# Kernel tuning notes

Measured on AMD Instinct MI355X. Metric: run time of the kernel, lower is better.

Reference implementation:

```python
import jax, jax.numpy as jnp
import numpy as np

B = 2
T = 1024
D_MODEL = 1024
EXPAND = 2
D_INNER = D_MODEL * EXPAND  # 2048
D_STATE = 16
D_CONV = 4
DT_RANK = 64  # ceil(1024/16)


def setup_inputs() -> dict:
    key = jax.random.key(0)
    ks = jax.random.split(key, 9)
    s = 0.02
    x = jax.random.normal(ks[0], (B, T, D_MODEL), jnp.float32)
    in_proj_w = jax.random.normal(ks[1], (2 * D_INNER, D_MODEL), jnp.float32) * s
    conv_w = jax.random.normal(ks[2], (D_INNER, 1, D_CONV), jnp.float32) * 0.1
    conv_b = jax.random.normal(ks[3], (D_INNER,), jnp.float32) * 0.01
    x_proj_w = jax.random.normal(ks[4], (DT_RANK + 2 * D_STATE, D_INNER), jnp.float32) * s
    dt_proj_w = jax.random.normal(ks[5], (D_INNER, DT_RANK), jnp.float32) * s
    dt_proj_b = jax.random.uniform(ks[6], (D_INNER,), jnp.float32, -4.0, -2.0)
    A_log = jnp.log(jnp.tile(jnp.arange(1, D_STATE + 1, dtype=jnp.float32), (D_INNER, 1)))
    D_param = jnp.ones((D_INNER,), jnp.float32)
    out_proj_w = jax.random.normal(ks[7], (D_MODEL, D_INNER), jnp.float32) * s
    return {"x": x, "in_proj_w": in_proj_w, "conv_w": conv_w, "conv_b": conv_b,
            "x_proj_w": x_proj_w, "dt_proj_w": dt_proj_w, "dt_proj_b": dt_proj_b,
            "A_log": A_log, "D_param": D_param, "out_proj_w": out_proj_w}


def reference(x, in_proj_w, conv_w, conv_b, x_proj_w, dt_proj_w, dt_proj_b,
              A_log, D_param, out_proj_w):
    Bsz, Tlen, _ = x.shape
    # input projection -> (B,T,2*d_inner); split into x-branch and gate z
    xz = jnp.einsum('btd,ed->bte', x, in_proj_w)
    xs, z = jnp.split(xz, 2, axis=-1)
    # causal depthwise conv1d: torch pads both sides by d_conv-1 then slices [:T],
    # equivalent to left-pad d_conv-1
    xc = jnp.swapaxes(xs, 1, 2)  # (B, d_inner, T)
    xc = jax.lax.conv_general_dilated(xc, conv_w, window_strides=(1,),
                                      padding=[(D_CONV - 1, 0)],
                                      feature_group_count=D_INNER)
    xc = xc + conv_b[None, :, None]
    xs = jax.nn.silu(jnp.swapaxes(xc, 1, 2))  # (B,T,d_inner)
    A = -jnp.exp(A_log)  # (d_inner, d_state)
    x_dbl = jnp.einsum('bti,ei->bte', xs, x_proj_w)
    dt, Bv, Cv = jnp.split(x_dbl, [DT_RANK, DT_RANK + D_STATE], axis=-1)
    dt = jax.nn.softplus(jnp.einsum('btr,ir->bti', dt, dt_proj_w) + dt_proj_b)
    # selective scan: h_t = exp(dt_t*A)*h_{t-1} + (dt_t*x_t)*B_t ; y_t = <h_t, C_t>
    def step(h, inp):
        dt_t, B_t, C_t, x_t = inp  # (B,Di),(B,Ds),(B,Ds),(B,Di)
        dA = jnp.exp(dt_t[:, :, None] * A[None])        # (B,Di,Ds)
        h = dA * h + (dt_t * x_t)[:, :, None] * B_t[:, None, :]
        y_t = jnp.einsum('bds,bs->bd', h, C_t)
        return h, y_t
    tm = lambda a: jnp.swapaxes(a, 0, 1)  # time-major
    h0 = jnp.zeros((Bsz, D_INNER, D_STATE), x.dtype)
    _, ys = jax.lax.scan(step, h0, (tm(dt), tm(Bv), tm(Cv), tm(xs)))
    y = jnp.swapaxes(ys, 0, 1) + xs * D_param  # (B,T,d_inner)
    y = y * jax.nn.silu(z)
    return jnp.einsum('bti,di->btd', y, out_proj_w)
```

## Files before the change

### kernel.cpp

```cpp
#include <hip/hip_runtime.h>
#include <hip/hip_bf16.h>
#include <math.h>

#define B_SZ 2
#define T_LEN 1024
#define DMODEL 1024
#define DINNER 2048
#define DSTATE 16
#define DCONV 4
#define DTRANK 64
#define MTOK (B_SZ * T_LEN)

#define NC 32
#define CLEN (T_LEN / NC)
#define NCH (B_SZ * DINNER)
#define NSTATES (NCH * DSTATE)

typedef __bf16 bf16x4 __attribute__((ext_vector_type(4)));
typedef __bf16 bf16x8 __attribute__((ext_vector_type(8)));
typedef float  f32x4  __attribute__((ext_vector_type(4)));

__device__ __forceinline__ float sigmoid_f(float v) { return 1.f / (1.f + __expf(-v)); }

__global__ __launch_bounds__(256) void convert_f32_bf16(const float* __restrict__ src,
                                                        __bf16* __restrict__ dst)
{
    const int i = blockIdx.x * blockDim.x + threadIdx.x;
    float4 a = reinterpret_cast<const float4*>(src)[2 * i];
    float4 b = reinterpret_cast<const float4*>(src)[2 * i + 1];
    bf16x8 o = {(__bf16)a.x, (__bf16)a.y, (__bf16)a.z, (__bf16)a.w,
                (__bf16)b.x, (__bf16)b.y, (__bf16)b.z, (__bf16)b.w};
    reinterpret_cast<bf16x8*>(dst)[i] = o;
}

template<int BN>
__global__ __launch_bounds__(256) void mfma_gemm_bf16(const __bf16* __restrict__ A, int lda,
                                                      const __bf16* __restrict__ Bm, int ldb,
                                                      float* __restrict__ C, int ldc, int K)
{
    constexpr int NF = BN / 32;
    constexpr int BCALLS = BN / 32;
    __shared__ __align__(16) __bf16 As[128 * 64];
    __shared__ __align__(16) __bf16 Bs[BN * 64];
    const int tid  = threadIdx.x;
    const int lane = tid & 63;
    const int w    = tid >> 6;
    const int wr   = w >> 1, wc = w & 1;
    const int m0   = blockIdx.y * 128, n0 = blockIdx.x * BN;

    f32x4 acc[4][NF];
    #pragma unroll
    for (int i = 0; i < 4; ++i)
        #pragma unroll
        for (int j = 0; j < NF; ++j) {
            f32x4 z = {0.f, 0.f, 0.f, 0.f};
            acc[i][j] = z;
        }

    const int fr = lane & 15;
    const int kq = (lane >> 4) * 8;

    for (int k0 = 0; k0 < K; k0 += 64) {
        #pragma unroll
        for (int c = 0; c < 4; ++c) {
            const int idx = c * 256 + tid;
            const int row = idx >> 3;
            const int kc  = (idx & 7) * 8;
            __builtin_amdgcn_global_load_lds(
                (const __attribute__((address_space(1))) unsigned int*)(A + (size_t)(m0 + row) * lda + k0 + kc),
                (__attribute__((address_space(3))) unsigned int*)(As + idx * 8),
                16, 0, 0);
        }
        #pragma unroll
        for (int c = 0; c < BCALLS; ++c) {
            const int idx = c * 256 + tid;
            const int row = idx >> 3;
            const int kc  = (idx & 7) * 8;
            __builtin_amdgcn_global_load_lds(
                (const __attribute__((address_space(1))) unsigned int*)(Bm + (size_t)(n0 + row) * ldb + k0 + kc),
                (__attribute__((address_space(3))) unsigned int*)(Bs + idx * 8),
                16, 0, 0);
        }
        __syncthreads();

        bf16x8 af[4][2], bfr[NF][2];
        #pragma unroll
        for (int i = 0; i < 4; ++i) {
            const __bf16* pa = As + (wr * 64 + i * 16 + fr) * 64 + kq;
            af[i][0] = *reinterpret_cast<const bf16x8*>(pa);
            af[i][1] = *reinterpret_cast<const bf16x8*>(pa + 32);
        }
        #pragma unroll
        for (int j = 0; j < NF; ++j) {
            const __bf16* pb = Bs + (wc * (BN / 2) + j * 16 + fr) * 64 + kq;
            bfr[j][0] = *reinterpret_cast<const bf16x8*>(pb);
            bfr[j][1] = *reinterpret_cast<const bf16x8*>(pb + 32);
        }
        #pragma unroll
        for (int i = 0; i < 4; ++i)
            #pragma unroll
            for (int j = 0; j < NF; ++j) {
                acc[i][j] = __builtin_amdgcn_mfma_f32_16x16x32_bf16(af[i][0], bfr[j][0], acc[i][j], 0, 0, 0);
                acc[i][j] = __builtin_amdgcn_mfma_f32_16x16x32_bf16(af[i][1], bfr[j][1], acc[i][j], 0, 0, 0);
            }
        __syncthreads();
    }

    const int crow = (lane >> 4) * 4;
    const int ccol = lane & 15;
    #pragma unroll
    for (int i = 0; i < 4; ++i)
        #pragma unroll
        for (int j = 0; j < NF; ++j) {
            float* cp = C + (size_t)(m0 + wr * 64 + i * 16 + crow) * ldc
                          + n0 + wc * (BN / 2) + j * 16 + ccol;
            cp[0 * ldc] = acc[i][j][0];
            cp[1 * ldc] = acc[i][j][1];
            cp[2 * ldc] = acc[i][j][2];
            cp[3 * ldc] = acc[i][j][3];
        }
}

template<int EPI>
__global__ __launch_bounds__(256) void gemm_nt(const float* __restrict__ A, int lda,
                                               const float* __restrict__ Bm, int ldb,
                                               float* __restrict__ C, int ldc,
                                               int M, int N, int K,
                                               const float* __restrict__ bias)
{
    __shared__ float As[16][68];
    __shared__ float Bs[16][68];
    const int tx = threadIdx.x & 15;
    const int ty = threadIdx.x >> 4;
    const int m0 = blockIdx.y * 64;
    const int n0 = blockIdx.x * 64;
    const int lr = threadIdx.x >> 2;
    const int lc = (threadIdx.x & 3) * 4;

    float acc[4][4] = {};

    for (int k0 = 0; k0 < K; k0 += 16) {
        {
            int m = m0 + lr;
            float4 v = make_float4(0.f, 0.f, 0.f, 0.f);
            if (m < M) v = *reinterpret_cast<const float4*>(&A[(size_t)m * lda + k0 + lc]);
            As[lc + 0][lr] = v.x; As[lc + 1][lr] = v.y;
            As[lc + 2][lr] = v.z; As[lc + 3][lr] = v.w;
        }
        {
            int n = n0 + lr;
            float4 v = make_float4(0.f, 0.f, 0.f, 0.f);
            if (n < N) v = *reinterpret_cast<const float4*>(&Bm[(size_t)n * ldb + k0 + lc]);
            Bs[lc + 0][lr] = v.x; Bs[lc + 1][lr] = v.y;
            Bs[lc + 2][lr] = v.z; Bs[lc + 3][lr] = v.w;
        }
        __syncthreads();
        #pragma unroll
        for (int kk = 0; kk < 16; ++kk) {
            float av[4], bv[4];
            #pragma unroll
            for (int i = 0; i < 4; ++i) av[i] = As[kk][ty + 16 * i];
            #pragma unroll
            for (int j = 0; j < 4; ++j) bv[j] = Bs[kk][tx + 16 * j];
            #pragma unroll
            for (int i = 0; i < 4; ++i)
                #pragma unroll
                for (int j = 0; j < 4; ++j)
                    acc[i][j] = fmaf(av[i], bv[j], acc[i][j]);
        }
        __syncthreads();
    }

    #pragma unroll
    for (int i = 0; i < 4; ++i) {
        int m = m0 + ty + 16 * i;
        if (m >= M) continue;
        #pragma unroll
        for (int j = 0; j < 4; ++j) {
            int n = n0 + tx + 16 * j;
            if (n >= N) continue;
            float v = acc[i][j];
            if (EPI == 1) {
                v += bias[n];
                v = (v > 20.f) ? v : log1pf(__expf(v));
            }
            C[(size_t)m * ldc + n] = v;
        }
    }
}

#define XP_KS 16
#define XP_KC (DINNER / XP_KS)

__global__ __launch_bounds__(256) void gemm_xproj_splitk(const float* __restrict__ xs,
                                                         const float* __restrict__ W,
                                                         float* __restrict__ pbuf)
{
    __shared__ float As[16][68];
    __shared__ float Bs[16][68];
    const int tx = threadIdx.x & 15;
    const int ty = threadIdx.x >> 4;
    const int n0 = blockIdx.x * 64;
    const int m0 = blockIdx.y * 64;
    const int kz = blockIdx.z;
    const int lr = threadIdx.x >> 2;
    const int lc = (threadIdx.x & 3) * 4;

    float acc[4][4] = {};

    for (int k0 = kz * XP_KC; k0 < (kz + 1) * XP_KC; k0 += 16) {
        {
            float4 v = *reinterpret_cast<const float4*>(&xs[(size_t)(m0 + lr) * DINNER + k0 + lc]);
            As[lc + 0][lr] = v.x; As[lc + 1][lr] = v.y;
            As[lc + 2][lr] = v.z; As[lc + 3][lr] = v.w;
        }
        {
            int n = n0 + lr;
            float4 v = make_float4(0.f, 0.f, 0.f, 0.f);
            if (n < DTRANK + 2 * DSTATE)
                v = *reinterpret_cast<const float4*>(&W[(size_t)n * DINNER + k0 + lc]);
            Bs[lc + 0][lr] = v.x; Bs[lc + 1][lr] = v.y;
            Bs[lc + 2][lr] = v.z; Bs[lc + 3][lr] = v.w;
        }
        __syncthreads();
        #pragma unroll
        for (int kk = 0; kk < 16; ++kk) {
            float av[4], bv[4];
            #pragma unroll
            for (int i = 0; i < 4; ++i) av[i] = As[kk][ty + 16 * i];
            #pragma unroll
            for (int j = 0; j < 4; ++j) bv[j] = Bs[kk][tx + 16 * j];
            #pragma unroll
            for (int i = 0; i < 4; ++i)
                #pragma unroll
                for (int j = 0; j < 4; ++j)
                    acc[i][j] = fmaf(av[i], bv[j], acc[i][j]);
        }
        __syncthreads();
    }

    float* pc = pbuf + (size_t)kz * MTOK * 96;
    #pragma unroll
    for (int i = 0; i < 4; ++i) {
        int m = m0 + ty + 16 * i;
        #pragma unroll
        for (int j = 0; j < 4; ++j) {
            int n = n0 + tx + 16 * j;
            if (n < 96) pc[(size_t)m * 96 + n] = acc[i][j];
        }
    }
}

__global__ __launch_bounds__(256) void reduce_xproj(const float* __restrict__ pbuf,
                                                    float* __restrict__ xdbl)
{
    const int idx = blockIdx.x * blockDim.x + threadIdx.x;
    const float4* p = reinterpret_cast<const float4*>(pbuf) + idx;
    float4 s = p[0];
    #pragma unroll
    for (int z = 1; z < XP_KS; ++z) {
        float4 v = p[(size_t)z * (MTOK * 96 / 4)];
        s.x += v.x; s.y += v.y; s.z += v.z; s.w += v.w;
    }
    reinterpret_cast<float4*>(xdbl)[idx] = s;
}

__global__ __launch_bounds__(256) void conv_silu_kernel(const float* __restrict__ xz,
                                                        const float* __restrict__ cw,
                                                        const float* __restrict__ cb,
                                                        float* __restrict__ xs)
{
    int tid = blockIdx.x * blockDim.x + threadIdx.x;
    int d = tid & (DINNER - 1);
    int t = (tid >> 11) & (T_LEN - 1);
    int b = tid >> 21;
    float acc = cb[d];
    const float4 w = *reinterpret_cast<const float4*>(&cw[d * DCONV]);
    float wv[4] = {w.x, w.y, w.z, w.w};
    #pragma unroll
    for (int j = 0; j < DCONV; ++j) {
        int tt = t - (DCONV - 1) + j;
        if (tt >= 0)
            acc = fmaf(xz[((size_t)(b * T_LEN + tt)) * (2 * DINNER) + d], wv[j], acc);
    }
    xs[tid] = acc * sigmoid_f(acc);
}

__global__ __launch_bounds__(256) void scan_pass1(const float* __restrict__ dt,
                                                  const float* __restrict__ xs,
                                                  const float* __restrict__ xdbl,
                                                  const float* __restrict__ A_log,
                                                  float* __restrict__ Pb,
                                                  float* __restrict__ Bb)
{
    __shared__ float sB[CLEN][16];
    const int tid = threadIdx.x;
    const int g   = blockIdx.x * 256 + tid;
    const int c   = blockIdx.y;
    const int b   = g >> 11;
    const int d   = g & (DINNER - 1);
    const int m0  = b * T_LEN + c * CLEN;

    if (tid < CLEN * 4) {
        int t = tid >> 2, s4 = (tid & 3) * 4;
        *reinterpret_cast<float4*>(&sB[t][s4]) =
            *reinterpret_cast<const float4*>(&xdbl[(size_t)(m0 + t) * 96 + DTRANK + s4]);
    }
    __syncthreads();

    float a[DSTATE], h[DSTATE];
    #pragma unroll
    for (int s4 = 0; s4 < DSTATE; s4 += 4) {
        float4 v = *reinterpret_cast<const float4*>(&A_log[d * DSTATE + s4]);
        a[s4 + 0] = -__expf(v.x); a[s4 + 1] = -__expf(v.y);
        a[s4 + 2] = -__expf(v.z); a[s4 + 3] = -__expf(v.w);
        h[s4 + 0] = 0.f; h[s4 + 1] = 0.f; h[s4 + 2] = 0.f; h[s4 + 3] = 0.f;
    }

    float sumdt = 0.f;
    float dtc = dt[(size_t)m0 * DINNER + d];
    float xc  = xs[(size_t)m0 * DINNER + d];
    for (int t = 0; t < CLEN; ++t) {
        float dtn = 0.f, xn = 0.f;
        if (t + 1 < CLEN) {
            dtn = dt[(size_t)(m0 + t + 1) * DINNER + d];
            xn  = xs[(size_t)(m0 + t + 1) * DINNER + d];
        }
        sumdt += dtc;
        const float u = dtc * xc;
        #pragma unroll
        for (int s = 0; s < DSTATE; ++s) {
            const float dA = __expf(dtc * a[s]);
            h[s] = fmaf(dA, h[s], u * sB[t][s]);
        }
        dtc = dtn; xc = xn;
    }

    float* pp = Pb + ((size_t)c * NCH + g) * DSTATE;
    float* bp = Bb + ((size_t)c * NCH + g) * DSTATE;
    #pragma unroll
    for (int s4 = 0; s4 < DSTATE; s4 += 4) {
        float4 pv = {__expf(a[s4] * sumdt), __expf(a[s4 + 1] * sumdt),
                     __expf(a[s4 + 2] * sumdt), __expf(a[s4 + 3] * sumdt)};
        *reinterpret_cast<float4*>(pp + s4) = pv;
        float4 hv = {h[s4], h[s4 + 1], h[s4 + 2], h[s4 + 3]};
        *reinterpret_cast<float4*>(bp + s4) = hv;
    }
}

__global__ __launch_bounds__(256) void scan_pass2(const float* __restrict__ Pb,
                                                  float* __restrict__ Bb)
{
    const int idx = blockIdx.x * blockDim.x + threadIdx.x;
    float h = 0.f;
    #pragma unroll
    for (int c = 0; c < NC; ++c) {
        const size_t o = (size_t)c * NSTATES + idx;
        const float P  = Pb[o];
        const float Bv = Bb[o];
        Bb[o] = h;
        h = fmaf(P, h, Bv);
    }
}

__global__ __launch_bounds__(256) void scan_pass3(const float* __restrict__ dt,
                                                  const float* __restrict__ xs,
                                                  const float* __restrict__ xdbl,
                                                  const float* __restrict__ Hs,
                                                  const float* __restrict__ A_log,
                                                  const float* __restrict__ Dp,
                                                  const float* __restrict__ xz,
                                                  __bf16* __restrict__ yMb)
{
    __shared__ float sBC[CLEN][32];
    const int tid = threadIdx.x;
    const int g   = blockIdx.x * 256 + tid;
    const int c   = blockIdx.y;
    const int b   = g >> 11;
    const int d   = g & (DINNER - 1);
    const int m0  = b * T_LEN + c * CLEN;

    {
        int t = tid >> 3, col = (tid & 7) * 4;
        if (t < CLEN)
            *reinterpret_cast<float4*>(&sBC[t][col]) =
                *reinterpret_cast<const float4*>(&xdbl[(size_t)(m0 + t) * 96 + DTRANK + col]);
    }
    __syncthreads();

    float a[DSTATE], h[DSTATE];
    #pragma unroll
    for (int s4 = 0; s4 < DSTATE; s4 += 4) {
        float4 v = *reinterpret_cast<const float4*>(&A_log[d * DSTATE + s4]);
        a[s4 + 0] = -__expf(v.x); a[s4 + 1] = -__expf(v.y);
        a[s4 + 2] = -__expf(v.z); a[s4 + 3] = -__expf(v.w);
        float4 hv = *reinterpret_cast<const float4*>(
            Hs + ((size_t)c * NCH + g) * DSTATE + s4);
        h[s4 + 0] = hv.x; h[s4 + 1] = hv.y; h[s4 + 2] = hv.z; h[s4 + 3] = hv.w;
    }
    const float Dv = Dp[d];

    float dtc = dt[(size_t)m0 * DINNER + d];
    float xc  = xs[(size_t)m0 * DINNER + d];
    float zc  = xz[(size_t)m0 * (2 * DINNER) + DINNER + d];
    for (int t = 0; t < CLEN; ++t) {
        float dtn = 0.f, xn = 0.f, zn = 0.f;
        if (t + 1 < CLEN) {
            dtn = dt[(size_t)(m0 + t + 1) * DINNER + d];
            xn  = xs[(size_t)(m0 + t + 1) * DINNER + d];
            zn  = xz[(size_t)(m0 + t + 1) * (2 * DINNER) + DINNER + d];
        }
        const float u = dtc * xc;
        float y0 = 0.f, y1 = 0.f, y2 = 0.f, y3 = 0.f;
        #pragma unroll
        for (int s = 0; s < DSTATE; s += 4) {
            float dA0 = __expf(dtc * a[s + 0]);
            float dA1 = __expf(dtc * a[s + 1]);
            float dA2 = __expf(dtc * a[s + 2]);
            float dA3 = __expf(dtc * a[s + 3]);
            h[s + 0] = fmaf(dA0, h[s + 0], u * sBC[t][s + 0]);
            h[s + 1] = fmaf(dA1, h[s + 1], u * sBC[t][s + 1]);
            h[s + 2] = fmaf(dA2, h[s + 2], u * sBC[t][s + 2]);
            h[s + 3] = fmaf(dA3, h[s + 3], u * sBC[t][s + 3]);
            y0 = fmaf(h[s + 0], sBC[t][16 + s + 0], y0);
            y1 = fmaf(h[s + 1], sBC[t][16 + s + 1], y1);
            y2 = fmaf(h[s + 2], sBC[t][16 + s + 2], y2);
            y3 = fmaf(h[s + 3], sBC[t][16 + s + 3], y3);
        }
        float y = (y0 + y1) + (y2 + y3) + xc * Dv;
        const float gate = zc * sigmoid_f(zc);
        yMb[(size_t)(m0 + t) * DINNER + d] = (__bf16)(y * gate);
        dtc = dtn; xc = xn; zc = zn;
    }
}

extern "C" void kernel_launch(void* const* d_in, const int* in_sizes, int n_in,
                              void* d_out, int out_size, void* d_ws, size_t ws_size,
                              hipStream_t stream) {
    const float* x         = (const float*)d_in[0];
    const float* in_proj_w = (const float*)d_in[1];
    const float* conv_w    = (const float*)d_in[2];
    const float* conv_b    = (const float*)d_in[3];
    const float* x_proj_w  = (const float*)d_in[4];
    const float* dt_proj_w = (const float*)d_in[5];
    const float* dt_proj_b = (const float*)d_in[6];
    const float* A_log     = (const float*)d_in[7];
    const float* D_param   = (const float*)d_in[8];
    const float* out_proj_w= (const float*)d_in[9];
    float* out = (float*)d_out;

    float* ws   = (float*)d_ws;
    const size_t M1 = (size_t)1024 * 1024;
    float*  xz     = ws;
    float*  xs     = ws + 8 * M1;
    __bf16* xb     = (__bf16*)(ws + 8 * M1);
    __bf16* wb_in  = (__bf16*)(ws + 9 * M1);
    float*  dt     = ws + 12 * M1;
    __bf16* wb_out = (__bf16*)(ws + 12 * M1);
    float*  pbuf   = ws + 16 * M1;
    float*  Pb     = ws + 16 * M1;
    float*  Bb     = ws + 18 * M1;
    __bf16* yMb    = (__bf16*)(ws + 16 * M1);
    float*  xdbl   = ws + 20 * M1;

    dim3 blk(256);

    convert_f32_bf16<<<dim3(MTOK * DMODEL / 8 / 256), blk, 0, stream>>>(x, xb);
    convert_f32_bf16<<<dim3(2 * DINNER * DMODEL / 8 / 256), blk, 0, stream>>>(in_proj_w, wb_in);

    mfma_gemm_bf16<128><<<dim3((2 * DINNER) / 128, MTOK / 128), blk, 0, stream>>>(
        xb, DMODEL, wb_in, DMODEL, xz, 2 * DINNER, DMODEL);

    conv_silu_kernel<<<dim3(B_SZ * T_LEN * DINNER / 256), blk, 0, stream>>>(xz, conv_w, conv_b, xs);

    gemm_xproj_splitk<<<dim3(2, MTOK / 64, XP_KS), blk, 0, stream>>>(xs, x_proj_w, pbuf);

    reduce_xproj<<<dim3(MTOK * 96 / 4 / 256), blk, 0, stream>>>(pbuf, xdbl);

    gemm_nt<1><<<dim3(DINNER / 64, MTOK / 64), blk, 0, stream>>>(
        xdbl, 96, dt_proj_w, DTRANK, dt, DINNER, MTOK, DINNER, DTRANK, dt_proj_b);

    scan_pass1<<<dim3(NCH / 256, NC), blk, 0, stream>>>(dt, xs, xdbl, A_log, Pb, Bb);
    scan_pass2<<<dim3(NSTATES / 256), blk, 0, stream>>>(Pb, Bb);
    scan_pass3<<<dim3(NCH / 256, NC), blk, 0, stream>>>(dt, xs, xdbl, Bb, A_log, D_param, xz, yMb);

    convert_f32_bf16<<<dim3(DMODEL * DINNER / 8 / 256), blk, 0, stream>>>(out_proj_w, wb_out);

    mfma_gemm_bf16<64><<<dim3(DMODEL / 64, MTOK / 128), blk, 0, stream>>>(
        yMb, DINNER, wb_out, DINNER, out, DMODEL, DINNER);
}
```

Before: 202.9 us.

## Store intermediates in bf16 and merge the three conversion kernels

```diff
diff --git a/kernel.cpp b/kernel.cpp
--- a/kernel.cpp
+++ b/kernel.cpp
@@ -22,21 +22,29 @@
 
 __device__ __forceinline__ float sigmoid_f(float v) { return 1.f / (1.f + __expf(-v)); }
 
-__global__ __launch_bounds__(256) void convert_f32_bf16(const float* __restrict__ src,
-                                                        __bf16* __restrict__ dst)
-{
-    const int i = blockIdx.x * blockDim.x + threadIdx.x;
-    float4 a = reinterpret_cast<const float4*>(src)[2 * i];
-    float4 b = reinterpret_cast<const float4*>(src)[2 * i + 1];
-    bf16x8 o = {(__bf16)a.x, (__bf16)a.y, (__bf16)a.z, (__bf16)a.w,
+__global__ __launch_bounds__(256) void convert3(const float* __restrict__ x,
+                                                const float* __restrict__ w_in,
+                                                const float* __restrict__ w_out,
+                                                __bf16* __restrict__ xb,
+                                                __bf16* __restrict__ wb_in,
+                                                __bf16* __restrict__ wb_out)
+{
+    const int gi = blockIdx.x * blockDim.x + threadIdx.x;
+    const float* src; __bf16* dst; int o;
+    if (gi < 262144)            { src = x;     dst = xb;     o = gi; }
+    else if (gi < 786432)       { src = w_in;  dst = wb_in;  o = gi - 262144; }
+    else                        { src = w_out; dst = wb_out; o = gi - 786432; }
+    float4 a = reinterpret_cast<const float4*>(src)[2 * o];
+    float4 b = reinterpret_cast<const float4*>(src)[2 * o + 1];
+    bf16x8 v = {(__bf16)a.x, (__bf16)a.y, (__bf16)a.z, (__bf16)a.w,
                 (__bf16)b.x, (__bf16)b.y, (__bf16)b.z, (__bf16)b.w};
-    reinterpret_cast<bf16x8*>(dst)[i] = o;
-}
-
-template<int BN>
+    reinterpret_cast<bf16x8*>(dst)[o] = v;
+}
+
+template<int BN, typename CT>
 __global__ __launch_bounds__(256) void mfma_gemm_bf16(const __bf16* __restrict__ A, int lda,
                                                       const __bf16* __restrict__ Bm, int ldb,
-                                                      float* __restrict__ C, int ldc, int K)
+                                                      CT* __restrict__ C, int ldc, int K)
 {
     constexpr int NF = BN / 32;
     constexpr int BCALLS = BN / 32;
@@ -112,21 +120,19 @@
     for (int i = 0; i < 4; ++i)
         #pragma unroll
         for (int j = 0; j < NF; ++j) {
-            float* cp = C + (size_t)(m0 + wr * 64 + i * 16 + crow) * ldc
-                          + n0 + wc * (BN / 2) + j * 16 + ccol;
-            cp[0 * ldc] = acc[i][j][0];
-            cp[1 * ldc] = acc[i][j][1];
-            cp[2 * ldc] = acc[i][j][2];
-            cp[3 * ldc] = acc[i][j][3];
-        }
-}
-
-template<int EPI>
-__global__ __launch_bounds__(256) void gemm_nt(const float* __restrict__ A, int lda,
-                                               const float* __restrict__ Bm, int ldb,
-                                               float* __restrict__ C, int ldc,
-                                               int M, int N, int K,
-                                               const float* __restrict__ bias)
+            CT* cp = C + (size_t)(m0 + wr * 64 + i * 16 + crow) * ldc
+                       + n0 + wc * (BN / 2) + j * 16 + ccol;
+            cp[0 * (size_t)ldc] = (CT)acc[i][j][0];
+            cp[1 * (size_t)ldc] = (CT)acc[i][j][1];
+            cp[2 * (size_t)ldc] = (CT)acc[i][j][2];
+            cp[3 * (size_t)ldc] = (CT)acc[i][j][3];
+        }
+}
+
+__global__ __launch_bounds__(256) void gemm_dtproj(const float* __restrict__ A,
+                                                   const float* __restrict__ Bm,
+                                                   __bf16* __restrict__ C,
+                                                   const float* __restrict__ bias)
 {
     __shared__ float As[16][68];
     __shared__ float Bs[16][68];
@@ -139,18 +145,14 @@
 
     float acc[4][4] = {};
 
-    for (int k0 = 0; k0 < K; k0 += 16) {
+    for (int k0 = 0; k0 < DTRANK; k0 += 16) {
         {
-            int m = m0 + lr;
-            float4 v = make_float4(0.f, 0.f, 0.f, 0.f);
-            if (m < M) v = *reinterpret_cast<const float4*>(&A[(size_t)m * lda + k0 + lc]);
+            float4 v = *reinterpret_cast<const float4*>(&A[(size_t)(m0 + lr) * 96 + k0 + lc]);
             As[lc + 0][lr] = v.x; As[lc + 1][lr] = v.y;
             As[lc + 2][lr] = v.z; As[lc + 3][lr] = v.w;
         }
         {
-            int n = n0 + lr;
-            float4 v = make_float4(0.f, 0.f, 0.f, 0.f);
-            if (n < N) v = *reinterpret_cast<const float4*>(&Bm[(size_t)n * ldb + k0 + lc]);
+            float4 v = *reinterpret_cast<const float4*>(&Bm[(size_t)(n0 + lr) * DTRANK + k0 + lc]);
             Bs[lc + 0][lr] = v.x; Bs[lc + 1][lr] = v.y;
             Bs[lc + 2][lr] = v.z; Bs[lc + 3][lr] = v.w;
         }
@@ -174,17 +176,12 @@
     #pragma unroll
     for (int i = 0; i < 4; ++i) {
         int m = m0 + ty + 16 * i;
-        if (m >= M) continue;
         #pragma unroll
         for (int j = 0; j < 4; ++j) {
             int n = n0 + tx + 16 * j;
-            if (n >= N) continue;
-            float v = acc[i][j];
-            if (EPI == 1) {
-                v += bias[n];
-                v = (v > 20.f) ? v : log1pf(__expf(v));
-            }
-            C[(size_t)m * ldc + n] = v;
+            float v = acc[i][j] + bias[n];
+            v = (v > 20.f) ? v : log1pf(__expf(v));
+            C[(size_t)m * DINNER + n] = (__bf16)v;
         }
     }
 }
@@ -192,7 +189,7 @@
 #define XP_KS 16
 #define XP_KC (DINNER / XP_KS)
 
-__global__ __launch_bounds__(256) void gemm_xproj_splitk(const float* __restrict__ xs,
+__global__ __launch_bounds__(256) void gemm_xproj_splitk(const __bf16* __restrict__ xsb,
                                                          const float* __restrict__ W,
                                                          float* __restrict__ pbuf)
 {
@@ -210,9 +207,9 @@
 
     for (int k0 = kz * XP_KC; k0 < (kz + 1) * XP_KC; k0 += 16) {
         {
-            float4 v = *reinterpret_cast<const float4*>(&xs[(size_t)(m0 + lr) * DINNER + k0 + lc]);
-            As[lc + 0][lr] = v.x; As[lc + 1][lr] = v.y;
-            As[lc + 2][lr] = v.z; As[lc + 3][lr] = v.w;
+            bf16x4 v = *reinterpret_cast<const bf16x4*>(&xsb[(size_t)(m0 + lr) * DINNER + k0 + lc]);
+            As[lc + 0][lr] = (float)v[0]; As[lc + 1][lr] = (float)v[1];
+            As[lc + 2][lr] = (float)v[2]; As[lc + 3][lr] = (float)v[3];
         }
         {
             int n = n0 + lr;
@@ -265,10 +262,10 @@
     reinterpret_cast<float4*>(xdbl)[idx] = s;
 }
 
-__global__ __launch_bounds__(256) void conv_silu_kernel(const float* __restrict__ xz,
+__global__ __launch_bounds__(256) void conv_silu_kernel(const __bf16* __restrict__ xzb,
                                                         const float* __restrict__ cw,
                                                         const float* __restrict__ cb,
-                                                        float* __restrict__ xs)
+                                                        __bf16* __restrict__ xsb)
 {
     int tid = blockIdx.x * blockDim.x + threadIdx.x;
     int d = tid & (DINNER - 1);
@@ -281,13 +278,13 @@
     for (int j = 0; j < DCONV; ++j) {
         int tt = t - (DCONV - 1) + j;
         if (tt >= 0)
-            acc = fmaf(xz[((size_t)(b * T_LEN + tt)) * (2 * DINNER) + d], wv[j], acc);
-    }
-    xs[tid] = acc * sigmoid_f(acc);
-}
-
-__global__ __launch_bounds__(256) void scan_pass1(const float* __restrict__ dt,
-                                                  const float* __restrict__ xs,
+            acc = fmaf((float)xzb[((size_t)(b * T_LEN + tt)) * (2 * DINNER) + d], wv[j], acc);
+    }
+    xsb[tid] = (__bf16)(acc * sigmoid_f(acc));
+}
+
+__global__ __launch_bounds__(256) void scan_pass1(const __bf16* __restrict__ dtb,
+                                                  const __bf16* __restrict__ xsb,
                                                   const float* __restrict__ xdbl,
                                                   const float* __restrict__ A_log,
                                                   float* __restrict__ Pb,
@@ -318,13 +315,13 @@
     }
 
     float sumdt = 0.f;
-    float dtc = dt[(size_t)m0 * DINNER + d];
-    float xc  = xs[(size_t)m0 * DINNER + d];
+    float dtc = (float)dtb[(size_t)m0 * DINNER + d];
+    float xc  = (float)xsb[(size_t)m0 * DINNER + d];
     for (int t = 0; t < CLEN; ++t) {
         float dtn = 0.f, xn = 0.f;
         if (t + 1 < CLEN) {
-            dtn = dt[(size_t)(m0 + t + 1) * DINNER + d];
-            xn  = xs[(size_t)(m0 + t + 1) * DINNER + d];
+            dtn = (float)dtb[(size_t)(m0 + t + 1) * DINNER + d];
+            xn  = (float)xsb[(size_t)(m0 + t + 1) * DINNER + d];
         }
         sumdt += dtc;
         const float u = dtc * xc;
@@ -363,13 +360,13 @@
     }
 }
 
-__global__ __launch_bounds__(256) void scan_pass3(const float* __restrict__ dt,
-                                                  const float* __restrict__ xs,
+__global__ __launch_bounds__(256) void scan_pass3(const __bf16* __restrict__ dtb,
+                                                  const __bf16* __restrict__ xsb,
                                                   const float* __restrict__ xdbl,
                                                   const float* __restrict__ Hs,
                                                   const float* __restrict__ A_log,
                                                   const float* __restrict__ Dp,
-                                                  const float* __restrict__ xz,
+                                                  const __bf16* __restrict__ xzb,
                                                   __bf16* __restrict__ yMb)
 {
     __shared__ float sBC[CLEN][32];
@@ -400,15 +397,15 @@
     }
     const float Dv = Dp[d];
 
-    float dtc = dt[(size_t)m0 * DINNER + d];
-    float xc  = xs[(size_t)m0 * DINNER + d];
-    float zc  = xz[(size_t)m0 * (2 * DINNER) + DINNER + d];
+    float dtc = (float)dtb[(size_t)m0 * DINNER + d];
+    float xc  = (float)xsb[(size_t)m0 * DINNER + d];
+    float zc  = (float)xzb[(size_t)m0 * (2 * DINNER) + DINNER + d];
     for (int t = 0; t < CLEN; ++t) {
         float dtn = 0.f, xn = 0.f, zn = 0.f;
         if (t + 1 < CLEN) {
-            dtn = dt[(size_t)(m0 + t + 1) * DINNER + d];
-            xn  = xs[(size_t)(m0 + t + 1) * DINNER + d];
-            zn  = xz[(size_t)(m0 + t + 1) * (2 * DINNER) + DINNER + d];
+            dtn = (float)dtb[(size_t)(m0 + t + 1) * DINNER + d];
+            xn  = (float)xsb[(size_t)(m0 + t + 1) * DINNER + d];
+            zn  = (float)xzb[(size_t)(m0 + t + 1) * (2 * DINNER) + DINNER + d];
         }
         const float u = dtc * xc;
         float y0 = 0.f, y1 = 0.f, y2 = 0.f, y3 = 0.f;
@@ -449,43 +446,39 @@
     const float* out_proj_w= (const float*)d_in[9];
     float* out = (float*)d_out;
 
-    float* ws   = (float*)d_ws;
+    float* ws = (float*)d_ws;
     const size_t M1 = (size_t)1024 * 1024;
-    float*  xz     = ws;
-    float*  xs     = ws + 8 * M1;
-    __bf16* xb     = (__bf16*)(ws + 8 * M1);
-    __bf16* wb_in  = (__bf16*)(ws + 9 * M1);
-    float*  dt     = ws + 12 * M1;
-    __bf16* wb_out = (__bf16*)(ws + 12 * M1);
-    float*  pbuf   = ws + 16 * M1;
+    __bf16* xzb    = (__bf16*)ws;
+    __bf16* xb     = (__bf16*)(ws + 4 * M1);
+    __bf16* wb_in  = (__bf16*)(ws + 5 * M1);
+    __bf16* wb_out = (__bf16*)(ws + 7 * M1);
+    __bf16* xsb    = (__bf16*)(ws + 8 * M1);
+    __bf16* dtb    = (__bf16*)(ws + 10 * M1);
+    float*  xdbl   = ws + 12 * M1;
+    float*  pbuf   = ws + 13 * M1;
     float*  Pb     = ws + 16 * M1;
     float*  Bb     = ws + 18 * M1;
-    __bf16* yMb    = (__bf16*)(ws + 16 * M1);
-    float*  xdbl   = ws + 20 * M1;
+    __bf16* yMb    = (__bf16*)(ws + 20 * M1);
 
     dim3 blk(256);
 
-    convert_f32_bf16<<<dim3(MTOK * DMODEL / 8 / 256), blk, 0, stream>>>(x, xb);
-    convert_f32_bf16<<<dim3(2 * DINNER * DMODEL / 8 / 256), blk, 0, stream>>>(in_proj_w, wb_in);
-
-    mfma_gemm_bf16<128><<<dim3((2 * DINNER) / 128, MTOK / 128), blk, 0, stream>>>(
-        xb, DMODEL, wb_in, DMODEL, xz, 2 * DINNER, DMODEL);
-
-    conv_silu_kernel<<<dim3(B_SZ * T_LEN * DINNER / 256), blk, 0, stream>>>(xz, conv_w, conv_b, xs);
-
-    gemm_xproj_splitk<<<dim3(2, MTOK / 64, XP_KS), blk, 0, stream>>>(xs, x_proj_w, pbuf);
+    convert3<<<dim3(4096), blk, 0, stream>>>(x, in_proj_w, out_proj_w, xb, wb_in, wb_out);
+
+    mfma_gemm_bf16<128, __bf16><<<dim3((2 * DINNER) / 128, MTOK / 128), blk, 0, stream>>>(
+        xb, DMODEL, wb_in, DMODEL, xzb, 2 * DINNER, DMODEL);
+
+    conv_silu_kernel<<<dim3(B_SZ * T_LEN * DINNER / 256), blk, 0, stream>>>(xzb, conv_w, conv_b, xsb);
+
+    gemm_xproj_splitk<<<dim3(2, MTOK / 64, XP_KS), blk, 0, stream>>>(xsb, x_proj_w, pbuf);
 
     reduce_xproj<<<dim3(MTOK * 96 / 4 / 256), blk, 0, stream>>>(pbuf, xdbl);
 
-    gemm_nt<1><<<dim3(DINNER / 64, MTOK / 64), blk, 0, stream>>>(
-        xdbl, 96, dt_proj_w, DTRANK, dt, DINNER, MTOK, DINNER, DTRANK, dt_proj_b);
-
-    scan_pass1<<<dim3(NCH / 256, NC), blk, 0, stream>>>(dt, xs, xdbl, A_log, Pb, Bb);
+    gemm_dtproj<<<dim3(DINNER / 64, MTOK / 64), blk, 0, stream>>>(xdbl, dt_proj_w, dtb, dt_proj_b);
+
+    scan_pass1<<<dim3(NCH / 256, NC), blk, 0, stream>>>(dtb, xsb, xdbl, A_log, Pb, Bb);
     scan_pass2<<<dim3(NSTATES / 256), blk, 0, stream>>>(Pb, Bb);
-    scan_pass3<<<dim3(NCH / 256, NC), blk, 0, stream>>>(dt, xs, xdbl, Bb, A_log, D_param, xz, yMb);
-
-    convert_f32_bf16<<<dim3(DMODEL * DINNER / 8 / 256), blk, 0, stream>>>(out_proj_w, wb_out);
-
-    mfma_gemm_bf16<64><<<dim3(DMODEL / 64, MTOK / 128), blk, 0, stream>>>(
+    scan_pass3<<<dim3(NCH / 256, NC), blk, 0, stream>>>(dtb, xsb, xdbl, Bb, A_log, D_param, xzb, yMb);
+
+    mfma_gemm_bf16<64, float><<<dim3(DMODEL / 64, MTOK / 128), blk, 0, stream>>>(
         yMb, DINNER, wb_out, DINNER, out, DMODEL, DINNER);
 }
```

Measured after the change: 194.2 us. 4.3% less time.
